# Optimization experiments

Hardware: AMD Instinct MI355X
Metric: run time of the kernel (lower is better)

The kernel has to match this reference:

```python
import jax, jax.numpy as jnp
import numpy as np
import math

B, S, D = 4, 2048, 1024

def setup_inputs() -> dict:
    key = jax.random.key(0)
    k1, k2, k3, k4 = jax.random.split(key, 4)
    scale = 1.0 / math.sqrt(D)
    return {
        "x": jax.random.normal(k1, (B, S, D), dtype=jnp.float32),
        "w_q": jax.random.normal(k2, (D, D), dtype=jnp.float32) * scale,
        "w_k": jax.random.normal(k3, (D, D), dtype=jnp.float32) * scale,
        "w_v": jax.random.normal(k4, (D, D), dtype=jnp.float32) * scale,
        "causal": 1,
    }

def reference(x, w_q, w_k, w_v, causal):
    # QKV projections: nn.Linear(dim, dim, bias=False) -> x @ W.T
    q = jnp.einsum('bsd,ed->bse', x, w_q)
    k = jnp.einsum('bsd,ed->bse', x, w_k)
    v = jnp.einsum('bsd,ed->bse', x, w_v)
    d_k = q.shape[-1]
    scores = jnp.einsum('bqd,bkd->bqk', q, k) / jnp.sqrt(jnp.asarray(d_k, q.dtype))
    if causal:
        seq_len = q.shape[-2]
        mask = jnp.triu(jnp.ones((seq_len, seq_len), dtype=bool), k=1)
        scores = jnp.where(mask, jnp.asarray(-jnp.inf, scores.dtype), scores)
    weights = jax.nn.softmax(scores, axis=-1)
    return jnp.einsum('bqk,bkd->bqd', weights, v)
```

## Files before the change

### kernel.cpp

```cpp
#include <hip/hip_runtime.h>
#include <stdint.h>

typedef unsigned short u16;
typedef __attribute__((ext_vector_type(8))) __bf16 bf16x8;
typedef __attribute__((ext_vector_type(4))) float f32x4;

__device__ __forceinline__ u16 f2bf(float f) {
  unsigned u = __float_as_uint(f);
  u += 0x7FFF + ((u >> 16) & 1);
  return (u16)(u >> 16);
}

__device__ __forceinline__ float bf2f(u16 h) {
  return __uint_as_float(((unsigned)h) << 16);
}

__device__ __forceinline__ void llds16(const u16* g, u16* l) {
  __builtin_amdgcn_global_load_lds(
      (const __attribute__((address_space(1))) void*)g,
      (__attribute__((address_space(3))) void*)l, 16, 0, 0);
}

__global__ __launch_bounds__(256) void cast_all(
    const float* __restrict__ x, const float* __restrict__ wq,
    const float* __restrict__ wk, const float* __restrict__ wv,
    u16* __restrict__ xb, u16* __restrict__ wb, float* __restrict__ lsum) {
  int i = blockIdx.x * 256 + threadIdx.x;
  if (i < 8192) lsum[i] = 0.f;
  const float* src; u16* dst; int off;
  if (i < 2097152)      { src = x;  dst = xb;            off = i; }
  else if (i < 2359296) { src = wq; dst = wb;            off = i - 2097152; }
  else if (i < 2621440) { src = wk; dst = wb + 1048576;  off = i - 2359296; }
  else                  { src = wv; dst = wb + 2097152;  off = i - 2621440; }
  float4 f = ((const float4*)src)[off];
  ushort4 o;
  o.x = f2bf(f.x); o.y = f2bf(f.y); o.z = f2bf(f.z); o.w = f2bf(f.w);
  ((ushort4*)dst)[off] = o;
}

template<int MODE>
__global__ __launch_bounds__(256) void gemm_nt(
    const u16* __restrict__ A, long long sA, int lda,
    const u16* __restrict__ B, long long sB, int ldb,
    void* __restrict__ Cp, long long sC, int ldc,
    int K, u16* __restrict__ vt, float scale,
    float* __restrict__ lsum, const int* __restrict__ causalp) {
  const int t = threadIdx.x;
  const int causal = (MODE == 0) ? 1 : causalp[0];

  int rt = blockIdx.x, ct = blockIdx.y;
  if (MODE == 1) {
    int x = blockIdx.x;
    if (x < 136) {
      int r = (int)((sqrtf(8.0f * x + 1.0f) - 1.0f) * 0.5f);
      while ((r + 1) * (r + 2) / 2 <= x) ++r;
      while (r * (r + 1) / 2 > x) --r;
      rt = r; ct = x - r * (r + 1) / 2;
    } else {
      int y = x - 136;
      int r = (int)((sqrtf(8.0f * y + 1.0f) - 1.0f) * 0.5f);
      while ((r + 1) * (r + 2) / 2 <= y) ++r;
      while (r * (r + 1) / 2 > y) --r;
      int c = y - r * (r + 1) / 2;
      rt = c; ct = r + 1;
      if (causal) return;
    }
  }
  if (MODE == 2) rt = 15 - blockIdx.x;

  const int rowbase = rt * 128;
  const int colbase = ct * 128;
  const u16* Ab = A + (long long)blockIdx.z * sA;
  const u16* Bb = B + (long long)blockIdx.z * sB;

  int Keff = K;
  if (MODE == 2 && causal) Keff = min(K, rowbase + 128);

  __shared__ u16 As[8192];
  __shared__ u16 Bs[8192];

  const int lane = t & 63;
  const int wv = t >> 6;
  const int wr = wv >> 1;
  const int wc = wv & 1;
  const int quad = lane >> 4;
  const int lr = lane & 15;

  f32x4 acc[4][4];
  const f32x4 zero = {0.f, 0.f, 0.f, 0.f};
#pragma unroll
  for (int i = 0; i < 4; ++i)
#pragma unroll
    for (int j = 0; j < 4; ++j) acc[i][j] = zero;

  {
    const int csw = (t & 7) ^ ((t >> 3) & 7);
    const u16* ga = Ab + (long long)(rowbase + (t >> 3)) * lda + csw * 8;
    const u16* gb = Bb + (long long)(colbase + (t >> 3)) * ldb + csw * 8;
    const long long ra = 32LL * lda, rb = 32LL * ldb;
    u16* la = As + t * 8;
    u16* lb = Bs + t * 8;

    const int m7 = lr & 7;
    const int a_base = (wr * 64 + lr) * 64 + ((quad ^ m7) * 8);
    const int b_base = (wc * 64 + lr) * 64 + ((quad ^ m7) * 8);

    for (int k0 = 0; k0 < Keff; k0 += 64) {
      __syncthreads();
#pragma unroll
      for (int i = 0; i < 4; ++i) {
        llds16(ga + k0 + i * ra, la + i * 2048);
        llds16(gb + k0 + i * rb, lb + i * 2048);
      }
      __syncthreads();
#pragma unroll
      for (int ks = 0; ks < 2; ++ks) {
        const int ko = ks ? 32 : 0;
        bf16x8 af[4], bfv[4];
#pragma unroll
        for (int tm = 0; tm < 4; ++tm)
          af[tm] = *(const bf16x8*)(As + ((a_base + tm * 1024) ^ ko));
#pragma unroll
        for (int tn = 0; tn < 4; ++tn)
          bfv[tn] = *(const bf16x8*)(Bs + ((b_base + tn * 1024) ^ ko));
#pragma unroll
        for (int tm = 0; tm < 4; ++tm)
#pragma unroll
          for (int tn = 0; tn < 4; ++tn)
            acc[tm][tn] = __builtin_amdgcn_mfma_f32_16x16x32_bf16(
                af[tm], bfv[tn], acc[tm][tn], 0, 0, 0);
      }
    }
  }

  if (MODE == 0 && colbase >= 2048) {
#pragma unroll
    for (int tm = 0; tm < 4; ++tm) {
      int s0 = rowbase + wr * 64 + tm * 16 + quad * 4;
      int b = s0 >> 11;
      int sl = s0 & 2047;
#pragma unroll
      for (int tn = 0; tn < 4; ++tn) {
        int e = colbase - 2048 + wc * 64 + tn * 16 + lr;
        ushort4 o;
        o.x = f2bf(acc[tm][tn][0]);
        o.y = f2bf(acc[tm][tn][1]);
        o.z = f2bf(acc[tm][tn][2]);
        o.w = f2bf(acc[tm][tn][3]);
        *(ushort4*)(vt + ((long long)(b * 1024 + e)) * 2048 + sl) = o;
      }
    }
    return;
  }

#pragma unroll
  for (int tm = 0; tm < 4; ++tm) {
#pragma unroll
    for (int r = 0; r < 4; ++r) {
      const int grow = rowbase + wr * 64 + tm * 16 + quad * 4 + r;
      float li, rsum = 0.f;
      if (MODE == 2) li = __builtin_amdgcn_rcpf(lsum[blockIdx.z * 2048 + grow]);
#pragma unroll
      for (int tn = 0; tn < 4; ++tn) {
        const int gcol = colbase + wc * 64 + tn * 16 + lr;
        float val = acc[tm][tn][r];
        if (MODE == 0) {
          ((u16*)Cp)[(long long)grow * ldc + gcol] = f2bf(val);
        } else if (MODE == 1) {
          u16* C = (u16*)Cp + (long long)blockIdx.z * sC;
          float ex = (causal && gcol > grow) ? 0.f : __expf(val * scale);
          C[(long long)grow * ldc + gcol] = f2bf(ex);
          rsum += ex;
        } else {
          float* C = (float*)Cp + (long long)blockIdx.z * sC;
          C[(long long)grow * ldc + gcol] = val * li;
        }
      }
      if (MODE == 1) {
#pragma unroll
        for (int o = 8; o > 0; o >>= 1) rsum += __shfl_xor(rsum, o, 64);
        if (lr == 0)
          atomicAdd(&lsum[blockIdx.z * 2048 + grow], rsum);
      }
    }
  }
}

extern "C" void kernel_launch(void* const* d_in, const int* in_sizes, int n_in,
                              void* d_out, int out_size, void* d_ws, size_t ws_size,
                              hipStream_t stream) {
  const float* x  = (const float*)d_in[0];
  const float* wq = (const float*)d_in[1];
  const float* wk = (const float*)d_in[2];
  const float* wv = (const float*)d_in[3];
  const int* causal = (const int*)d_in[4];
  float* out = (float*)d_out;

  char* ws = (char*)d_ws;
  u16* xb = (u16*)(ws);
  u16* wb = (u16*)(ws + 16777216);
  u16* qk = (u16*)(ws + 23068672);
  u16* vt = (u16*)(ws + 56623104);
  u16* sb = (u16*)(ws + 73400320);
  float* lsum = (float*)(ws + 106954752);

  cast_all<<<11264, 256, 0, stream>>>(x, wq, wk, wv, xb, wb, lsum);

  gemm_nt<0><<<dim3(64, 24, 1), 256, 0, stream>>>(
      xb, 0, 1024, wb, 0, 1024, qk, 0, 2048, 1024, vt, 1.0f, nullptr, causal);

  gemm_nt<1><<<dim3(256, 1, 4), 256, 0, stream>>>(
      qk, 2048LL * 2048, 2048, qk + 1024, 2048LL * 2048, 2048,
      sb, 2048LL * 2048, 2048, 1024, nullptr, 0.03125f, lsum, causal);

  gemm_nt<2><<<dim3(16, 8, 4), 256, 0, stream>>>(
      sb, 2048LL * 2048, 2048, vt, 1024LL * 2048, 2048,
      out, 2048LL * 1024, 1024, 2048, nullptr, 1.0f, lsum, causal);
}
```

Baseline: 236.6 us.

## Replace QKV projection GEMM with 256x256-tile, 8-wave software-pipelined kernel

Adds a dedicated QKV projection kernel that uses 256x256 output tiles with 512 threads per block. It double-buffers shared memory with asynchronous global-to-LDS loads issued in interleaved phases and explicit vmcnt waits, and raises MFMA priority with setprio. The aim is to hide global-load latency behind MFMA work and to improve data reuse per tile over the previous 128x128 single-buffered kernel. In exchange it uses 128KB of LDS per block and far more accumulator registers, and the K loop is hard-coded for K=1024.

```diff
diff --git a/kernel.cpp b/kernel.cpp
--- a/kernel.cpp
+++ b/kernel.cpp
@@ -37,6 +37,148 @@
   o.x = f2bf(f.x); o.y = f2bf(f.y); o.z = f2bf(f.z); o.w = f2bf(f.w);
   ((ushort4*)dst)[off] = o;
 }
+
+#define VM8 asm volatile("s_waitcnt vmcnt(8)" ::: "memory")
+#define VM4 asm volatile("s_waitcnt vmcnt(4)" ::: "memory")
+#define VM0 asm volatile("s_waitcnt vmcnt(0)" ::: "memory")
+#define VMN ((void)0)
+
+#define STGA(P, KH, KOFF) do {                                              \
+  llds16(gA + (KOFF),          As + (P)*16384 + (KH)*8192 + t*8);           \
+  llds16(gA + (KOFF) + 131072, As + (P)*16384 + (KH)*8192 + 4096 + t*8);    \
+} while (0)
+
+#define STGB(P, KH, KOFF) do {                                              \
+  llds16(gB + (KOFF),          Bs + (P)*16384 + (KH)*8192 + t*8);           \
+  llds16(gB + (KOFF) + 131072, Bs + (P)*16384 + (KH)*8192 + 4096 + t*8);    \
+} while (0)
+
+#define PH(P, KH, MH, RDB, VMW, ...) do {                                   \
+  bf16x8 af[4];                                                             \
+  { const int ab_ = (P)*16384 + (KH)*8192 + (wr*64 + (MH)*32)*64 + fr_off;  \
+    af[0] = *(const bf16x8*)(As + ab_);                                     \
+    af[1] = *(const bf16x8*)(As + ab_ + 512);                               \
+    af[2] = *(const bf16x8*)(As + ab_ + 1024);                              \
+    af[3] = *(const bf16x8*)(As + ab_ + 1536); }                            \
+  if (RDB) {                                                                \
+    const int bb_ = (P)*16384 + (KH)*8192 + (wc*32)*64 + fr_off;            \
+    bfv[0] = *(const bf16x8*)(Bs + bb_);                                    \
+    bfv[1] = *(const bf16x8*)(Bs + bb_ + 512);                              \
+    bfv[2] = *(const bf16x8*)(Bs + bb_ + 1024);                             \
+    bfv[3] = *(const bf16x8*)(Bs + bb_ + 1536); }                           \
+  __VA_ARGS__;                                                              \
+  asm volatile("" ::: "memory");                                            \
+  __builtin_amdgcn_sched_barrier(0);                                        \
+  __builtin_amdgcn_s_barrier();                                             \
+  asm volatile("s_waitcnt lgkmcnt(0)" ::: "memory");                        \
+  __builtin_amdgcn_sched_barrier(0);                                        \
+  __builtin_amdgcn_s_setprio(1);                                            \
+  _Pragma("unroll")                                                         \
+  for (int m_ = 0; m_ < 4; ++m_) {                                          \
+    _Pragma("unroll")                                                       \
+    for (int n_ = 0; n_ < 4; ++n_)                                          \
+      acc[(MH)*4 + m_][n_] = __builtin_amdgcn_mfma_f32_16x16x32_bf16(       \
+          af[m_], bfv[n_], acc[(MH)*4 + m_][n_], 0, 0, 0);                  \
+  }                                                                         \
+  __builtin_amdgcn_s_setprio(0);                                            \
+  __builtin_amdgcn_sched_barrier(0);                                        \
+  VMW;                                                                      \
+  asm volatile("" ::: "memory");                                            \
+  __builtin_amdgcn_s_barrier();                                             \
+  asm volatile("" ::: "memory");                                            \
+  __builtin_amdgcn_sched_barrier(0);                                        \
+} while (0)
+
+__global__ __launch_bounds__(512, 2) void gemm_qkv(
+    const u16* __restrict__ A, const u16* __restrict__ B,
+    u16* __restrict__ qk, u16* __restrict__ vt) {
+  __shared__ u16 As[32768];
+  __shared__ u16 Bs[32768];
+  const int t = threadIdx.x;
+  const int lane = t & 63;
+  const int wr = (t >> 6) >> 2;
+  const int wc = (t >> 6) & 3;
+  const int lr = lane & 15;
+  const int q  = lane >> 4;
+  const int fr_off = (lr >> 1) * 64 + ((((lr & 1) << 2) | q) ^ (lr >> 1)) * 8;
+  const int rowbase = blockIdx.x << 8;
+  const int colbase = blockIdx.y << 8;
+
+  const int cc = (t & 7) ^ ((t >> 3) & 7);
+  const u16* gA = A + (long long)(rowbase + ((t >> 3) << 1) + (cc >> 2)) * 1024
+                    + (cc & 3) * 8;
+  const u16* gB = B + (long long)(colbase + ((t >> 3) << 1) + (cc >> 2)) * 1024
+                    + (cc & 3) * 8;
+
+  f32x4 acc[8][4];
+  const f32x4 z = {0.f, 0.f, 0.f, 0.f};
+#pragma unroll
+  for (int i = 0; i < 8; ++i)
+#pragma unroll
+    for (int j = 0; j < 4; ++j) acc[i][j] = z;
+  bf16x8 bfv[4];
+
+  STGA(0, 0, 0);  STGB(0, 0, 0);
+  STGA(0, 1, 32); STGB(0, 1, 32);
+  STGA(1, 0, 64); STGB(1, 0, 64);
+  VM8;
+  asm volatile("" ::: "memory");
+  __builtin_amdgcn_s_barrier();
+
+#pragma unroll 1
+  for (int tt = 0; tt < 7; ++tt) {
+    const int ka = tt * 128;
+    PH(0, 0, 0, 1, VMN, STGA(1, 1, ka + 96));
+    PH(0, 0, 1, 0, VM8, STGB(1, 1, ka + 96));
+    PH(0, 1, 0, 1, VMN, STGA(0, 0, ka + 128));
+    PH(0, 1, 1, 0, VM8, STGB(0, 0, ka + 128));
+    PH(1, 0, 0, 1, VMN, STGA(0, 1, ka + 160));
+    PH(1, 0, 1, 0, VM8, STGB(0, 1, ka + 160));
+    PH(1, 1, 0, 1, VMN, STGA(1, 0, ka + 192));
+    PH(1, 1, 1, 0, VM8, STGB(1, 0, ka + 192));
+  }
+  PH(0, 0, 0, 1, VMN, STGA(1, 1, 992));
+  PH(0, 0, 1, 0, VM8, STGB(1, 1, 992));
+  PH(0, 1, 0, 1, VMN);
+  PH(0, 1, 1, 0, VM4);
+  PH(1, 0, 0, 1, VMN);
+  PH(1, 0, 1, 0, VM0);
+  PH(1, 1, 0, 1, VMN);
+  PH(1, 1, 1, 0, VMN);
+
+  if (colbase >= 2048) {
+#pragma unroll
+    for (int mi = 0; mi < 8; ++mi) {
+      const int s0 = rowbase + wr * 128 + mi * 16 + q * 4;
+      const int b = s0 >> 11, sl = s0 & 2047;
+#pragma unroll
+      for (int n = 0; n < 4; ++n) {
+        const int e = colbase - 2048 + wc * 64 + n * 16 + lr;
+        ushort4 o;
+        o.x = f2bf(acc[mi][n][0]); o.y = f2bf(acc[mi][n][1]);
+        o.z = f2bf(acc[mi][n][2]); o.w = f2bf(acc[mi][n][3]);
+        *(ushort4*)(vt + ((long long)(b * 1024 + e)) * 2048 + sl) = o;
+      }
+    }
+  } else {
+#pragma unroll
+    for (int mi = 0; mi < 8; ++mi) {
+#pragma unroll
+      for (int r = 0; r < 4; ++r) {
+        const long long grow = rowbase + wr * 128 + mi * 16 + q * 4 + r;
+#pragma unroll
+        for (int n = 0; n < 4; ++n) {
+          const int gcol = colbase + wc * 64 + n * 16 + lr;
+          qk[grow * 2048 + gcol] = f2bf(acc[mi][n][r]);
+        }
+      }
+    }
+  }
+}
+
+#undef PH
+#undef STGA
+#undef STGB
 
 template<int MODE>
 __global__ __launch_bounds__(256) void gemm_nt(
@@ -206,8 +348,7 @@
 
   cast_all<<<11264, 256, 0, stream>>>(x, wq, wk, wv, xb, wb, lsum);
 
-  gemm_nt<0><<<dim3(64, 24, 1), 256, 0, stream>>>(
-      xb, 0, 1024, wb, 0, 1024, qk, 0, 2048, 1024, vt, 1.0f, nullptr, causal);
+  gemm_qkv<<<dim3(32, 12, 1), 512, 0, stream>>>(xb, wb, qk, vt);
 
   gemm_nt<1><<<dim3(256, 1, 4), 256, 0, stream>>>(
       qk, 2048LL * 2048, 2048, qk + 1024, 2048LL * 2048, 2048,
```

Result: slower. 242.5 us (+2.5%).
